# Performance work log

Hardware: AMD Instinct MI355X
Metric: run time of the kernel (lower is better)

Reference implementation:

```python
import jax, jax.numpy as jnp
import numpy as np

N = 100000
E = 1600000
IN_C, HID_C, OUT_C = 128, 128, 64


def setup_inputs() -> dict:
    key = jax.random.key(0)
    ks = jax.random.split(key, 8)
    x = jax.random.normal(ks[0], (N, IN_C), dtype=jnp.float32)
    edge_index = jax.random.randint(ks[1], (2, E), 0, N, dtype=jnp.int64)
    s_in = 1.0 / np.sqrt(IN_C)
    s_hid = 1.0 / np.sqrt(HID_C)
    w1l = jax.random.uniform(ks[2], (HID_C, IN_C), jnp.float32, -s_in, s_in)
    w1r = jax.random.uniform(ks[3], (HID_C, IN_C), jnp.float32, -s_in, s_in)
    b1 = jnp.zeros((HID_C,), jnp.float32)
    w2l = jax.random.uniform(ks[4], (OUT_C, HID_C), jnp.float32, -s_hid, s_hid)
    w2r = jax.random.uniform(ks[5], (OUT_C, HID_C), jnp.float32, -s_hid, s_hid)
    b2 = jnp.zeros((OUT_C,), jnp.float32)
    return {"x": x, "edge_index": edge_index, "w1l": w1l, "w1r": w1r,
            "b1": b1, "w2l": w2l, "w2r": w2r, "b2": b2}


def _sage_conv(x, src, dst, wl, wr, b):
    # mean aggregation of neighbor messages x[src] at dst
    agg = jax.ops.segment_sum(x[src], dst, num_segments=N)  # [N, d]
    deg = jax.ops.segment_sum(jnp.ones((src.shape[0],), x.dtype), dst, num_segments=N)
    agg = agg / jnp.maximum(deg, 1.0)[:, None]
    # PyG SAGEConv: lin_l(agg) + lin_r(x); lin_l carries the bias
    return agg @ wl.T + b + x @ wr.T


def reference(x, edge_index, w1l, w1r, b1, w2l, w2r, b2):
    src, dst = edge_index[0], edge_index[1]
    h = jax.nn.relu(_sage_conv(x, src, dst, w1l, w1r, b1))
    z = _sage_conv(h, src, dst, w2l, w2r, b2)  # [N, OUT_C]
    # decode: gather node pairs, elementwise multiply + reduce -> [E]
    return jnp.sum(z[src] * z[dst], axis=1)
```

## Files before the change

kernel.cpp:

```cpp
#include <hip/hip_runtime.h>


#define IN_C      128
#define HID_C     128
#define OUT_C     64
#define NPART     8
#define NREP      4
#define SUBCAP    65536
#define BPB       8
#define EPB       1024
#define CAP       64

typedef unsigned short u16;
typedef __attribute__((ext_vector_type(8))) __bf16 bf16x8;
typedef __attribute__((ext_vector_type(4))) float f32x4;
typedef __attribute__((ext_vector_type(4))) int i32x4;
typedef __attribute__((ext_vector_type(2))) int i32x2;

__device__ inline u16 f2bf(float f) {
    unsigned u = __float_as_uint(f);
    u += 0x7fff + ((u >> 16) & 1);
    return (u16)(u >> 16);
}
__device__ inline float bflo(unsigned v) { return __uint_as_float(v << 16); }
__device__ inline float bfhi(unsigned v) { return __uint_as_float(v & 0xffff0000u); }

__global__ __launch_bounds__(256) void bucket_edges(const int* __restrict__ ei,
                                                    int* __restrict__ bcur,
                                                    i32x2* __restrict__ bkt,
                                                    int E, int n) {
    __shared__ int cnt8[NPART];
    __shared__ int gofs[NPART];
    const int tid = threadIdx.x;
    if (tid < NPART) cnt8[tid] = 0;
    __syncthreads();

    const int rep  = blockIdx.x & (NREP - 1);
    const int nr   = (n + NPART - 1) / NPART;
    const int base = blockIdx.x * EPB + tid * 4;

    i32x4 d4 = {-1, -1, -1, -1}, s4 = {0, 0, 0, 0};
    if (base < E) {
        d4 = __builtin_nontemporal_load((const i32x4*)(ei + (size_t)E + base));
        s4 = __builtin_nontemporal_load((const i32x4*)(ei + base));
    }

    int bk[4], rk[4];
#pragma unroll
    for (int j = 0; j < 4; ++j) {
        int d = d4[j], s = s4[j];
        bk[j] = ((unsigned)d < (unsigned)n && (unsigned)s < (unsigned)n)
                    ? (int)((unsigned)d / (unsigned)nr) : -1;
        if (bk[j] >= 0) rk[j] = atomicAdd(&cnt8[bk[j]], 1);
    }
    __syncthreads();
    if (tid < NPART) gofs[tid] = atomicAdd(&bcur[tid * NREP + rep], cnt8[tid]);
    __syncthreads();

#pragma unroll
    for (int j = 0; j < 4; ++j) {
        int b = bk[j];
        if (b >= 0) {
            int pos = gofs[b] + rk[j];
            if (pos < SUBCAP) {
                i32x2 v; v.x = s4[j]; v.y = d4[j];
                bkt[(size_t)(b * NREP + rep) * SUBCAP + pos] = v;
            }
        }
    }
}

__global__ __launch_bounds__(256) void fill_from_bkt(const i32x2* __restrict__ bkt,
                                                     const int* __restrict__ bcur,
                                                     int* __restrict__ cnt,
                                                     int* __restrict__ csr, int n) {
    const int b     = blockIdx.x & (NPART - 1);
    const int t     = blockIdx.x >> 3;
    const int r     = t & (NREP - 1);
    const int chunk = t >> 2;
    const int idx   = b * NREP + r;
    const int m     = min(bcur[idx], SUBCAP);
    const int per   = (m + BPB - 1) / BPB;
    const int lo    = chunk * per;
    const int hi    = min(m, lo + per);
    const i32x2* sp = bkt + (size_t)idx * SUBCAP;

    for (int i0 = lo + threadIdx.x * 4; i0 < hi; i0 += 1024) {
        int kmax = min(4, hi - i0);
        i32x2 ev[4];
#pragma unroll
        for (int k = 0; k < 4; ++k)
            if (k < kmax) ev[k] = __builtin_nontemporal_load(&sp[i0 + k]);
        int rk[4];
#pragma unroll
        for (int k = 0; k < 4; ++k)
            if (k < kmax) rk[k] = atomicAdd(&cnt[ev[k].y], 1);
#pragma unroll
        for (int k = 0; k < 4; ++k)
            if (k < kmax) {
                int rr = rk[k];
                if (rr < CAP) csr[(size_t)ev[k].y * CAP + rr] = ev[k].x;
            }
    }
}

__global__ __launch_bounds__(256) void deg_inv(const int* __restrict__ cnt,
                                               float* __restrict__ inv_deg, int n) {
    int i = blockIdx.x * 256 + threadIdx.x;
    if (i < n) inv_deg[i] = 1.0f / (float)max(cnt[i], 1);
}

__global__ __launch_bounds__(256) void cvt_x(const float* __restrict__ in,
                                             u16* __restrict__ outb, int n4) {
    int i = blockIdx.x * 256 + threadIdx.x;
    if (i >= n4) return;
    float4 v = ((const float4*)in)[i];
    ushort4 o;
    o.x = f2bf(v.x); o.y = f2bf(v.y); o.z = f2bf(v.z); o.w = f2bf(v.w);
    ((ushort4*)outb)[i] = o;
}

__global__ __launch_bounds__(256) void cvt_w(const float* __restrict__ w1l,
                                             const float* __restrict__ w1r,
                                             const float* __restrict__ w2l,
                                             const float* __restrict__ w2r,
                                             u16* __restrict__ Wb1,
                                             u16* __restrict__ Wb2) {
    int i = blockIdx.x * 256 + threadIdx.x;
    if (i < 32768) {
        int c = i >> 8, k = i & 255;
        float v = (k < 128) ? w1l[c * 128 + k] : w1r[c * 128 + (k - 128)];
        Wb1[i] = f2bf(v);
    } else if (i < 49152) {
        int j = i - 32768;
        float v = (j < 8192) ? w2l[j] : w2r[j - 8192];
        Wb2[j] = f2bf(v);
    }
}

__global__ __launch_bounds__(256) void gemm_l1(const u16* __restrict__ A0,
                                               const u16* __restrict__ A1,
                                               const u16* __restrict__ Wb,
                                               const float* __restrict__ bias,
                                               u16* __restrict__ outp, int nrows) {
    constexpr int K    = 256;
    constexpr int COLS = 128;
    constexpr int KS   = K / 32;
    constexpr int NCT  = COLS / 16;
    constexpr int WROW = K + 8;
    __shared__ u16 wl[COLS * WROW];

    const int t = threadIdx.x;
    for (int i = t; i < COLS * (K / 8); i += 256) {
        int r = i >> 5, p = i & 31;
        *(uint4*)&wl[r * WROW + p * 8] = *(const uint4*)&Wb[(size_t)r * K + p * 8];
    }
    __syncthreads();

    const int wv    = t >> 6;
    const int lane  = t & 63;
    const int cl    = lane & 15;
    const int quad  = lane >> 4;
    const int rbase = blockIdx.x * 128 + wv * 32;

    bf16x8 afrag[2][KS];
#pragma unroll
    for (int tile = 0; tile < 2; ++tile) {
        int r = min(rbase + tile * 16 + cl, nrows - 1);
        const u16* s0 = A0 + (size_t)r * 128 + quad * 8;
        const u16* s1 = A1 + (size_t)r * 128 + quad * 8;
#pragma unroll
        for (int ks = 0; ks < 4; ++ks) {
            afrag[tile][ks]     = *(const bf16x8*)(s0 + ks * 32);
            afrag[tile][4 + ks] = *(const bf16x8*)(s1 + ks * 32);
        }
    }

#pragma unroll
    for (int ct = 0; ct < NCT; ++ct) {
        f32x4 acc0 = {0.f, 0.f, 0.f, 0.f};
        f32x4 acc1 = {0.f, 0.f, 0.f, 0.f};
        const u16* wp = &wl[(ct * 16 + cl) * WROW + quad * 8];
#pragma unroll
        for (int ks = 0; ks < KS; ++ks) {
            bf16x8 bfrag = *(const bf16x8*)(wp + ks * 32);
            acc0 = __builtin_amdgcn_mfma_f32_16x16x32_bf16(afrag[0][ks], bfrag, acc0, 0, 0, 0);
            acc1 = __builtin_amdgcn_mfma_f32_16x16x32_bf16(afrag[1][ks], bfrag, acc1, 0, 0, 0);
        }
        int gc = ct * 16 + cl;
        float bv = bias[gc];
#pragma unroll
        for (int tile = 0; tile < 2; ++tile) {
            f32x4 a = tile ? acc1 : acc0;
#pragma unroll
            for (int r = 0; r < 4; ++r) {
                int row = rbase + tile * 16 + quad * 4 + r;
                if (row < nrows)
                    outp[(size_t)row * COLS + gc] = f2bf(fmaxf(a[r] + bv, 0.f));
            }
        }
    }
}

template <int K, int COLS>
__global__ __launch_bounds__(256) void gemm_mfma(const u16* __restrict__ xb,
                                                 const u16* __restrict__ Wb,
                                                 const float* __restrict__ bias,
                                                 u16* __restrict__ outA,
                                                 u16* __restrict__ outB,
                                                 int nrows) {
    constexpr int NCOL = 2 * COLS;
    constexpr int NCT  = NCOL / 16;
    constexpr int KS   = K / 32;
    constexpr int WROW = K + 8;
    __shared__ u16 wl[NCOL * WROW];

    const int t = threadIdx.x;
    for (int i = t; i < NCOL * (K / 8); i += 256) {
        int r = i / (K / 8), p = i % (K / 8);
        *(uint4*)&wl[r * WROW + p * 8] = *(const uint4*)&Wb[(size_t)r * K + p * 8];
    }
    __syncthreads();

    const int wv    = t >> 6;
    const int lane  = t & 63;
    const int cl    = lane & 15;
    const int quad  = lane >> 4;
    const int rbase = blockIdx.x * 128 + wv * 32;

    bf16x8 afrag[2][KS];
#pragma unroll
    for (int tile = 0; tile < 2; ++tile) {
        int r = rbase + tile * 16 + cl;
        const u16* src = xb + (size_t)min(r, nrows - 1) * K + quad * 8;
#pragma unroll
        for (int ks = 0; ks < KS; ++ks)
            afrag[tile][ks] = *(const bf16x8*)(src + ks * 32);
    }

#pragma unroll
    for (int ct = 0; ct < NCT; ++ct) {
        f32x4 acc0 = {0.f, 0.f, 0.f, 0.f};
        f32x4 acc1 = {0.f, 0.f, 0.f, 0.f};
        const u16* wp = &wl[(ct * 16 + cl) * WROW + quad * 8];
#pragma unroll
        for (int ks = 0; ks < KS; ++ks) {
            bf16x8 bfrag = *(const bf16x8*)(wp + ks * 32);
            acc0 = __builtin_amdgcn_mfma_f32_16x16x32_bf16(afrag[0][ks], bfrag, acc0, 0, 0, 0);
            acc1 = __builtin_amdgcn_mfma_f32_16x16x32_bf16(afrag[1][ks], bfrag, acc1, 0, 0, 0);
        }
        int gc = ct * 16 + cl;
        bool isA = gc < COLS;
        float bv = isA ? 0.f : bias[gc - COLS];
        u16* dst = isA ? (outA + gc) : (outB + (gc - COLS));
#pragma unroll
        for (int tile = 0; tile < 2; ++tile) {
            f32x4 a = tile ? acc1 : acc0;
#pragma unroll
            for (int r = 0; r < 4; ++r) {
                int row = rbase + tile * 16 + quad * 4 + r;
                if (row < nrows) dst[(size_t)row * COLS] = f2bf(a[r] + bv);
            }
        }
    }
}

template <int C, bool HAS_OTHER>
__global__ __launch_bounds__(256) void agg_bf(const u16* __restrict__ gl,
                                              const u16* __restrict__ other,
                                              const int* __restrict__ cnt,
                                              const int* __restrict__ csr,
                                              const float* __restrict__ inv_deg,
                                              u16* __restrict__ outp, int n) {
    constexpr int G = C / 8;
    int t = threadIdx.x;
    int node = blockIdx.x * (256 / G) + t / G;
    int l = t % G;
    if (node >= n) return;

    int deg = min(cnt[node], CAP);
    const int* sp = csr + (size_t)node * CAP;
    float a[8] = {0.f, 0.f, 0.f, 0.f, 0.f, 0.f, 0.f, 0.f};
    const size_t coff = (size_t)l * 8;
    for (int p = 0; p < deg; ++p) {
        int s = sp[p];
        uint4 v = *(const uint4*)(gl + (size_t)s * C + coff);
        a[0] += bflo(v.x); a[1] += bfhi(v.x);
        a[2] += bflo(v.y); a[3] += bfhi(v.y);
        a[4] += bflo(v.z); a[5] += bfhi(v.z);
        a[6] += bflo(v.w); a[7] += bfhi(v.w);
    }
    float id = inv_deg[node];
    float r[8];
    if (HAS_OTHER) {
        uint4 o = *(const uint4*)(other + (size_t)node * C + coff);
        r[0] = fmaf(a[0], id, bflo(o.x)); r[1] = fmaf(a[1], id, bfhi(o.x));
        r[2] = fmaf(a[2], id, bflo(o.y)); r[3] = fmaf(a[3], id, bfhi(o.y));
        r[4] = fmaf(a[4], id, bflo(o.z)); r[5] = fmaf(a[5], id, bfhi(o.z));
        r[6] = fmaf(a[6], id, bflo(o.w)); r[7] = fmaf(a[7], id, bfhi(o.w));
    } else {
#pragma unroll
        for (int j = 0; j < 8; ++j) r[j] = a[j] * id;
    }
    uint4 w;
    w.x = (unsigned)f2bf(r[0]) | ((unsigned)f2bf(r[1]) << 16);
    w.y = (unsigned)f2bf(r[2]) | ((unsigned)f2bf(r[3]) << 16);
    w.z = (unsigned)f2bf(r[4]) | ((unsigned)f2bf(r[5]) << 16);
    w.w = (unsigned)f2bf(r[6]) | ((unsigned)f2bf(r[7]) << 16);
    *(uint4*)(outp + (size_t)node * C + coff) = w;
}

__global__ __launch_bounds__(256) void decode(const u16* __restrict__ z,
                                              const int* __restrict__ ei,
                                              float* __restrict__ out, int E, int n) {
    int t = blockIdx.x * 256 + threadIdx.x;
    int e = t >> 3, l = t & 7;
    if (e >= E) return;
    int s = __builtin_nontemporal_load(ei + e);
    int d = __builtin_nontemporal_load(ei + (size_t)E + e);
    float p = 0.f;
    if ((unsigned)s < (unsigned)n && (unsigned)d < (unsigned)n) {
        uint4 a = *(const uint4*)(z + (size_t)s * OUT_C + l * 8);
        uint4 b = *(const uint4*)(z + (size_t)d * OUT_C + l * 8);
        p  = bflo(a.x) * bflo(b.x) + bfhi(a.x) * bfhi(b.x);
        p += bflo(a.y) * bflo(b.y) + bfhi(a.y) * bfhi(b.y);
        p += bflo(a.z) * bflo(b.z) + bfhi(a.z) * bfhi(b.z);
        p += bflo(a.w) * bflo(b.w) + bfhi(a.w) * bfhi(b.w);
    }
    p += __shfl_xor(p, 4);
    p += __shfl_xor(p, 2);
    p += __shfl_xor(p, 1);
    if (l == 0) out[e] = p;
}

extern "C" void kernel_launch(void* const* d_in, const int* in_sizes, int n_in,
                              void* d_out, int out_size, void* d_ws, size_t ws_size,
                              hipStream_t stream) {
    const float* x   = (const float*)d_in[0];
    const int*   ei  = (const int*)d_in[1];
    const float* w1l = (const float*)d_in[2];
    const float* w1r = (const float*)d_in[3];
    const float* b1  = (const float*)d_in[4];
    const float* w2l = (const float*)d_in[5];
    const float* w2r = (const float*)d_in[6];
    const float* b2  = (const float*)d_in[7];
    float*       out = (float*)d_out;

    const int N = in_sizes[0] / IN_C;
    const int E = in_sizes[1] / 2;

    auto alignup = [](size_t v) { return (v + 255) & ~(size_t)255; };
    char* p = (char*)d_ws;
    int*   cnt       = (int*)p;   p += alignup((size_t)N * 4);
    float* inv_deg   = (float*)p; p += alignup((size_t)N * 4);
    int*   bcur      = (int*)p;   p += alignup((size_t)NPART * NREP * 4);
    int*   csr       = (int*)p;   p += alignup((size_t)N * CAP * 4);
    i32x2* bkt       = (i32x2*)p; p += alignup((size_t)NPART * NREP * SUBCAP * 8);
    u16*   Wb1       = (u16*)p;   p += alignup((size_t)HID_C * 2 * IN_C * 2);
    u16*   Wb2       = (u16*)p;   p += alignup((size_t)2 * OUT_C * HID_C * 2);
    u16*   xb        = (u16*)p;   p += alignup((size_t)N * IN_C * 2);
    u16*   ag1       = (u16*)p;   p += alignup((size_t)N * HID_C * 2);
    u16*   hb        = (u16*)p;   p += alignup((size_t)N * HID_C * 2);
    u16*   hlb       = xb;
    u16*   hrb       = xb + (size_t)N * OUT_C;
    u16*   zb        = ag1;

    cvt_x<<<(N * IN_C / 4 + 255) / 256, 256, 0, stream>>>(x, xb, N * IN_C / 4);
    cvt_w<<<192, 256, 0, stream>>>(w1l, w1r, w2l, w2r, Wb1, Wb2);

    hipMemsetAsync(cnt, 0, (size_t)N * 4, stream);
    hipMemsetAsync(bcur, 0, (size_t)NPART * NREP * 4, stream);
    const int nblk1 = (E + EPB - 1) / EPB;
    bucket_edges<<<nblk1, 256, 0, stream>>>(ei, bcur, bkt, E, N);
    fill_from_bkt<<<NPART * NREP * BPB, 256, 0, stream>>>(bkt, bcur, cnt, csr, N);
    deg_inv<<<(N + 255) / 256, 256, 0, stream>>>(cnt, inv_deg, N);

    const int rb = (N + 127) / 128;

    agg_bf<HID_C, false><<<(N + 15) / 16, 256, 0, stream>>>(xb, nullptr, cnt, csr,
                                                            inv_deg, ag1, N);
    gemm_l1<<<rb, 256, 0, stream>>>(ag1, xb, Wb1, b1, hb, N);

    gemm_mfma<HID_C, OUT_C><<<rb, 256, 0, stream>>>(hb, Wb2, b2, hlb, hrb, N);
    agg_bf<OUT_C, true><<<(N + 31) / 32, 256, 0, stream>>>(hlb, hrb, cnt, csr,
                                                           inv_deg, zb, N);

    decode<<<((size_t)E * 8 + 255) / 256, 256, 0, stream>>>(zb, ei, out, E, N);
}
```

Measured before the change: 425.3 us.

## Batch neighbor gathers in aggregation and spread bucket counters across more replicas

The aggregation loop now loads four neighbor indices at once and issues up to four row gathers before accumulating, to increase memory-level parallelism in the bandwidth-bound gather. Edge bucketing doubles the replica count and pads each bucket counter to its own stride, to reduce atomic contention. The fill kernel uses more blocks per bucket. It also halves per-replica capacity, which relies on the edges spreading evenly.

```diff
diff --git a/kernel.cpp b/kernel.cpp
--- a/kernel.cpp
+++ b/kernel.cpp
@@ -5,9 +5,10 @@
 #define HID_C     128
 #define OUT_C     64
 #define NPART     8
-#define NREP      4
-#define SUBCAP    65536
-#define BPB       8
+#define NREP      8
+#define CSTRIDE   16
+#define SUBCAP    32768
+#define BPB       16
 #define EPB       1024
 #define CAP       64
 
@@ -54,7 +55,8 @@
         if (bk[j] >= 0) rk[j] = atomicAdd(&cnt8[bk[j]], 1);
     }
     __syncthreads();
-    if (tid < NPART) gofs[tid] = atomicAdd(&bcur[tid * NREP + rep], cnt8[tid]);
+    if (tid < NPART)
+        gofs[tid] = atomicAdd(&bcur[(tid * NREP + rep) * CSTRIDE], cnt8[tid]);
     __syncthreads();
 
 #pragma unroll
@@ -77,9 +79,9 @@
     const int b     = blockIdx.x & (NPART - 1);
     const int t     = blockIdx.x >> 3;
     const int r     = t & (NREP - 1);
-    const int chunk = t >> 2;
+    const int chunk = t >> 3;
     const int idx   = b * NREP + r;
-    const int m     = min(bcur[idx], SUBCAP);
+    const int m     = min(bcur[idx * CSTRIDE], SUBCAP);
     const int per   = (m + BPB - 1) / BPB;
     const int lo    = chunk * per;
     const int hi    = min(m, lo + per);
@@ -282,13 +284,21 @@
     const int* sp = csr + (size_t)node * CAP;
     float a[8] = {0.f, 0.f, 0.f, 0.f, 0.f, 0.f, 0.f, 0.f};
     const size_t coff = (size_t)l * 8;
-    for (int p = 0; p < deg; ++p) {
-        int s = sp[p];
-        uint4 v = *(const uint4*)(gl + (size_t)s * C + coff);
-        a[0] += bflo(v.x); a[1] += bfhi(v.x);
-        a[2] += bflo(v.y); a[3] += bfhi(v.y);
-        a[4] += bflo(v.z); a[5] += bfhi(v.z);
-        a[6] += bflo(v.w); a[7] += bfhi(v.w);
+    for (int p0 = 0; p0 < deg; p0 += 4) {
+        i32x4 s4 = *(const i32x4*)(sp + p0);
+        int kmax = min(4, deg - p0);
+        uint4 v[4];
+#pragma unroll
+        for (int k = 0; k < 4; ++k)
+            if (k < kmax) v[k] = *(const uint4*)(gl + (size_t)s4[k] * C + coff);
+#pragma unroll
+        for (int k = 0; k < 4; ++k)
+            if (k < kmax) {
+                a[0] += bflo(v[k].x); a[1] += bfhi(v[k].x);
+                a[2] += bflo(v[k].y); a[3] += bfhi(v[k].y);
+                a[4] += bflo(v[k].z); a[5] += bfhi(v[k].z);
+                a[6] += bflo(v[k].w); a[7] += bfhi(v[k].w);
+            }
     }
     float id = inv_deg[node];
     float r[8];
@@ -353,7 +363,7 @@
     char* p = (char*)d_ws;
     int*   cnt       = (int*)p;   p += alignup((size_t)N * 4);
     float* inv_deg   = (float*)p; p += alignup((size_t)N * 4);
-    int*   bcur      = (int*)p;   p += alignup((size_t)NPART * NREP * 4);
+    int*   bcur      = (int*)p;   p += alignup((size_t)NPART * NREP * CSTRIDE * 4);
     int*   csr       = (int*)p;   p += alignup((size_t)N * CAP * 4);
     i32x2* bkt       = (i32x2*)p; p += alignup((size_t)NPART * NREP * SUBCAP * 8);
     u16*   Wb1       = (u16*)p;   p += alignup((size_t)HID_C * 2 * IN_C * 2);
@@ -369,7 +379,7 @@
     cvt_w<<<192, 256, 0, stream>>>(w1l, w1r, w2l, w2r, Wb1, Wb2);
 
     hipMemsetAsync(cnt, 0, (size_t)N * 4, stream);
-    hipMemsetAsync(bcur, 0, (size_t)NPART * NREP * 4, stream);
+    hipMemsetAsync(bcur, 0, (size_t)NPART * NREP * CSTRIDE * 4, stream);
     const int nblk1 = (E + EPB - 1) / EPB;
     bucket_edges<<<nblk1, 256, 0, stream>>>(ei, bcur, bkt, E, N);
     fill_from_bkt<<<NPART * NREP * BPB, 256, 0, stream>>>(bkt, bcur, cnt, csr, N);
```

Result: faster. 399.2 us (-6.1%).
